# Kernel optimization log

Measured on AMD Instinct MI355X. Metric: run time of the kernel, lower is better.

The kernel has to match this reference:

```python
import jax, jax.numpy as jnp
import numpy as np

NUM_EXPERTS = 16
IN_FEATURES = 512
OUT_FEATURES = 512
N_TOKENS = 2048


def setup_inputs() -> dict:
    key = jax.random.key(0)
    k_x, k_idx, k_w, k_b = jax.random.split(key, 4)
    x = jax.random.normal(k_x, (N_TOKENS, IN_FEATURES), dtype=jnp.float32)
    indices = jax.random.randint(k_idx, (N_TOKENS,), 0, NUM_EXPERTS, dtype=jnp.int64)
    # nn.Linear default init: U(-1/sqrt(in), 1/sqrt(in)) for weight [out,in] and bias [out]
    bound = 1.0 / np.sqrt(IN_FEATURES)
    W = jax.random.uniform(k_w, (NUM_EXPERTS, OUT_FEATURES, IN_FEATURES),
                           minval=-bound, maxval=bound, dtype=jnp.float32)
    b = jax.random.uniform(k_b, (NUM_EXPERTS, OUT_FEATURES),
                           minval=-bound, maxval=bound, dtype=jnp.float32)
    return {"x": x, "indices": indices, "W": W, "b": b}


def reference(x, indices, W, b):
    # Faithful to SwitchLinear.forward: gather per-token expert weight/bias,
    # then per-token GEMV (batched matmul with a length-1 row dim).
    w_tok = W[indices]            # [N, out, in]  (naive per-token weight gather)
    b_tok = b[indices]            # [N, out]
    out = jnp.einsum('ni,noi->no', x, w_tok) + b_tok  # [N, out]
    return out
```

## Files before the change

### kernel.cpp

```cpp
#include <hip/hip_runtime.h>
#include <hip/hip_bf16.h>

#define NE    16
#define INF   512
#define OUTF  512
#define NT    2048
#define OTILE 64
#define TCH   32
#define NZ    2
#define WROWS OTILE
#define LSTRIDE 520

#define SZ_W   (WROWS * LSTRIDE * 2)
#define SZ_X   (TCH * LSTRIDE * 2)
#define SZ_LST ((NT + TCH) * 4)
#define SMEM_BYTES (SZ_W + SZ_X + SZ_LST + 32)

typedef __attribute__((ext_vector_type(4))) float f32x4;
typedef __attribute__((ext_vector_type(8))) short bf16x8;
typedef __attribute__((ext_vector_type(4))) short bf16x4;

__device__ inline short f2bf(float f) {
    union { __hip_bfloat16 h; short s; } u;
    u.h = __float2bfloat16(f);
    return u.s;
}

__device__ inline bf16x4 cvt4(f32x4 v) {
    bf16x4 r;
    r[0] = f2bf(v[0]); r[1] = f2bf(v[1]); r[2] = f2bf(v[2]); r[3] = f2bf(v[3]);
    return r;
}

__global__ __launch_bounds__(512, 2)
void switch_linear_kernel(const float* __restrict__ x,
                          const int* __restrict__ idx,
                          const float* __restrict__ W,
                          const float* __restrict__ bias,
                          float* __restrict__ out)
{
    extern __shared__ char smem[];
    short* s_W    = (short*)smem;
    short* s_X    = (short*)(smem + SZ_W);
    int*   s_list = (int*)(smem + SZ_W + SZ_X);
    int*   s_wcnt = (int*)(smem + SZ_W + SZ_X + SZ_LST);

    const int b   = blockIdx.x;
    const int e   = b & 15;
    const int oj  = (b >> 4) & 7;
    const int o0  = oj * OTILE;
    const int z   = b >> 7;
    const int tid = threadIdx.x;
    const int lane = tid & 63;
    const int wid  = tid >> 6;

    int iv[4];
#pragma unroll
    for (int it = 0; it < 4; ++it)
        iv[it] = idx[wid * 256 + it * 64 + lane];

    const float* wbase = W + ((size_t)e * OUTF + o0) * INF;
#pragma unroll
    for (int i = 0; i < 16; ++i) {
        const int ii = z ? ((i + 8) & 15) : i;
        const int li = tid + ii * 512;
        f32x4 v = ((const f32x4*)wbase)[li];
        const int row = li >> 7;
        const int col = (li * 4) & 511;
        *(bf16x4*)(&s_W[row * LSTRIDE + col]) = cvt4(v);
    }

    unsigned long long masks[4];
    int wtot = 0;
#pragma unroll
    for (int it = 0; it < 4; ++it) {
        const unsigned long long mk = __ballot(iv[it] == e);
        masks[it] = mk;
        wtot += __popcll(mk);
    }
    if (lane == 0) s_wcnt[wid] = wtot;
    __syncthreads();
    int base = 0;
#pragma unroll
    for (int w = 0; w < 8; ++w) { int c = s_wcnt[w]; if (w < wid) base += c; }
    const int cnt = s_wcnt[0] + s_wcnt[1] + s_wcnt[2] + s_wcnt[3]
                  + s_wcnt[4] + s_wcnt[5] + s_wcnt[6] + s_wcnt[7];
    const unsigned long long below = (1ull << lane) - 1ull;
    int run = base;
#pragma unroll
    for (int it = 0; it < 4; ++it) {
        const unsigned long long mk = masks[it];
        if (mk & (1ull << lane))
            s_list[run + __popcll(mk & below)] = wid * 256 + it * 64 + lane;
        run += __popcll(mk);
    }
    const int cnt_pad = (cnt + TCH - 1) & ~(TCH - 1);
    for (int i = cnt + tid; i < cnt_pad; i += 512) s_list[i] = -1;
    __syncthreads();
    if (cnt == 0) return;

    const int wt = wid >> 2;
    const int wo = wid & 3;
    const int lr = lane & 15;
    const int q  = lane >> 4;
    const int orow = o0 + wo * 16 + lr;

    bf16x8 bfr[16];
#pragma unroll
    for (int kk = 0; kk < 16; ++kk)
        bfr[kk] = *(const bf16x8*)(&s_W[(wo * 16 + lr) * LSTRIDE + kk * 32 + q * 8]);
    const float bv = bias[e * OUTF + orow];

    const int slot = tid >> 4;
    const int sub  = tid & 15;

    const int M = (cnt_pad - z * TCH + (NZ * TCH) - 1) / (NZ * TCH);
    if (M > 0) {
        int m0 = oj % M;
        for (int k = 0; k < M; ++k) {
            int m = m0 + k; if (m >= M) m -= M;
            const int cb = z * TCH + m * (NZ * TCH);

            int tok_s = s_list[cb + slot];
            if (tok_s < 0) tok_s = 0;
            const f32x4* xr = (const f32x4*)(x + (size_t)tok_s * INF);
#pragma unroll
            for (int i = 0; i < 8; ++i) {
                f32x4 v = xr[sub + i * 16];
                *(bf16x4*)(&s_X[slot * LSTRIDE + sub * 4 + i * 64]) = cvt4(v);
            }
            __syncthreads();

            f32x4 acc = {0.f, 0.f, 0.f, 0.f};
#pragma unroll
            for (int kk = 0; kk < 16; ++kk) {
                bf16x8 afr = *(const bf16x8*)(&s_X[(wt * 16 + lr) * LSTRIDE + kk * 32 + q * 8]);
                acc = __builtin_amdgcn_mfma_f32_16x16x32_bf16(afr, bfr[kk], acc, 0, 0, 0);
            }
#pragma unroll
            for (int j = 0; j < 4; ++j) {
                const int tok = s_list[cb + wt * 16 + q * 4 + j];
                if (tok >= 0) out[(size_t)tok * OUTF + orow] = acc[j] + bv;
            }
            __syncthreads();
        }
    }
}

extern "C" void kernel_launch(void* const* d_in, const int* in_sizes, int n_in,
                              void* d_out, int out_size, void* d_ws, size_t ws_size,
                              hipStream_t stream) {
    const float* x    = (const float*)d_in[0];
    const int*   idx  = (const int*)d_in[1];
    const float* W    = (const float*)d_in[2];
    const float* bias = (const float*)d_in[3];
    float* out = (float*)d_out;

    dim3 grid(NE * (OUTF / OTILE) * NZ);
    dim3 block(512);
    switch_linear_kernel<<<grid, block, SMEM_BYTES, stream>>>(x, idx, W, bias, out);
}
```

Baseline: 13.29 us.

## Double token chunk to 64 and restructure wave tiling over outputs

Raises the token chunk per iteration from 32 to 64 and remaps the 8 waves to 4 token groups by 2 output halves, so each wave runs two MFMAs per k-step and reads weight fragments from LDS instead of holding them in registers. The weight tile load is issued to registers before the routing ballot and converted into LDS afterwards, overlapping global latency with list construction. The z-dependent rotation of the weight-load order is dropped, and the trailing barrier is skipped on the last iteration. The intent is fewer loop iterations and barriers per block, traded against more LDS traffic and extra register pressure from the wreg and xreg arrays.

```diff
diff --git a/kernel.cpp b/kernel.cpp
--- a/kernel.cpp
+++ b/kernel.cpp
@@ -6,29 +6,29 @@
 #define OUTF  512
 #define NT    2048
 #define OTILE 64
-#define TCH   32
+#define TCH   64
 #define NZ    2
-#define WROWS OTILE
 #define LSTRIDE 520
 
-#define SZ_W   (WROWS * LSTRIDE * 2)
+#define SZ_W   (OTILE * LSTRIDE * 2)
 #define SZ_X   (TCH * LSTRIDE * 2)
 #define SZ_LST ((NT + TCH) * 4)
-#define SMEM_BYTES (SZ_W + SZ_X + SZ_LST + 32)
+#define SMEM_BYTES (SZ_W + SZ_X + SZ_LST + 64)
 
 typedef __attribute__((ext_vector_type(4))) float f32x4;
 typedef __attribute__((ext_vector_type(8))) short bf16x8;
 typedef __attribute__((ext_vector_type(4))) short bf16x4;
 
-__device__ inline short f2bf(float f) {
-    union { __hip_bfloat16 h; short s; } u;
+__device__ inline unsigned short f2bf(float f) {
+    union { __hip_bfloat16 h; unsigned short s; } u;
     u.h = __float2bfloat16(f);
     return u.s;
 }
 
 __device__ inline bf16x4 cvt4(f32x4 v) {
     bf16x4 r;
-    r[0] = f2bf(v[0]); r[1] = f2bf(v[1]); r[2] = f2bf(v[2]); r[3] = f2bf(v[3]);
+    r[0] = (short)f2bf(v[0]); r[1] = (short)f2bf(v[1]);
+    r[2] = (short)f2bf(v[2]); r[3] = (short)f2bf(v[3]);
     return r;
 }
 
@@ -60,15 +60,10 @@
         iv[it] = idx[wid * 256 + it * 64 + lane];
 
     const float* wbase = W + ((size_t)e * OUTF + o0) * INF;
+    f32x4 wreg[16];
 #pragma unroll
-    for (int i = 0; i < 16; ++i) {
-        const int ii = z ? ((i + 8) & 15) : i;
-        const int li = tid + ii * 512;
-        f32x4 v = ((const f32x4*)wbase)[li];
-        const int row = li >> 7;
-        const int col = (li * 4) & 511;
-        *(bf16x4*)(&s_W[row * LSTRIDE + col]) = cvt4(v);
-    }
+    for (int i = 0; i < 16; ++i)
+        wreg[i] = ((const f32x4*)wbase)[tid + i * 512];
 
     unsigned long long masks[4];
     int wtot = 0;
@@ -96,54 +91,68 @@
     }
     const int cnt_pad = (cnt + TCH - 1) & ~(TCH - 1);
     for (int i = cnt + tid; i < cnt_pad; i += 512) s_list[i] = -1;
+
+#pragma unroll
+    for (int i = 0; i < 16; ++i) {
+        const int li  = tid + i * 512;
+        const int row = li >> 7;
+        const int col = (li * 4) & 511;
+        *(bf16x4*)(&s_W[row * LSTRIDE + col]) = cvt4(wreg[i]);
+    }
     __syncthreads();
     if (cnt == 0) return;
 
-    const int wt = wid >> 2;
-    const int wo = wid & 3;
-    const int lr = lane & 15;
-    const int q  = lane >> 4;
-    const int orow = o0 + wo * 16 + lr;
+    const int wt  = wid >> 1;
+    const int wo2 = wid & 1;
+    const int lr  = lane & 15;
+    const int q   = lane >> 4;
+    const int or0 = o0 + wo2 * 32 + lr;
+    const float bv0 = bias[e * OUTF + or0];
+    const float bv1 = bias[e * OUTF + or0 + 16];
 
-    bf16x8 bfr[16];
+    const int slot = tid >> 3;
+    const int sub  = tid & 7;
+
+    const int nch = cnt_pad / TCH;
+    const int M = (nch - z + NZ - 1) / NZ;
+    if (M <= 0) return;
+    int m0 = oj % M;
+
+    for (int k = 0; k < M; ++k) {
+        int m = m0 + k; if (m >= M) m -= M;
+        const int cb = (z + m * NZ) * TCH;
+
+        int tok_s = s_list[cb + slot];
+        if (tok_s < 0) tok_s = 0;
+        const f32x4* xr = (const f32x4*)(x + (size_t)tok_s * INF);
+        f32x4 xreg[16];
 #pragma unroll
-    for (int kk = 0; kk < 16; ++kk)
-        bfr[kk] = *(const bf16x8*)(&s_W[(wo * 16 + lr) * LSTRIDE + kk * 32 + q * 8]);
-    const float bv = bias[e * OUTF + orow];
+        for (int i = 0; i < 16; ++i)
+            xreg[i] = xr[sub + i * 8];
+#pragma unroll
+        for (int i = 0; i < 16; ++i)
+            *(bf16x4*)(&s_X[slot * LSTRIDE + (sub + i * 8) * 4]) = cvt4(xreg[i]);
+        __syncthreads();
 
-    const int slot = tid >> 4;
-    const int sub  = tid & 15;
-
-    const int M = (cnt_pad - z * TCH + (NZ * TCH) - 1) / (NZ * TCH);
-    if (M > 0) {
-        int m0 = oj % M;
-        for (int k = 0; k < M; ++k) {
-            int m = m0 + k; if (m >= M) m -= M;
-            const int cb = z * TCH + m * (NZ * TCH);
-
-            int tok_s = s_list[cb + slot];
-            if (tok_s < 0) tok_s = 0;
-            const f32x4* xr = (const f32x4*)(x + (size_t)tok_s * INF);
+        f32x4 acc0 = {0.f, 0.f, 0.f, 0.f};
+        f32x4 acc1 = {0.f, 0.f, 0.f, 0.f};
 #pragma unroll
-            for (int i = 0; i < 8; ++i) {
-                f32x4 v = xr[sub + i * 16];
-                *(bf16x4*)(&s_X[slot * LSTRIDE + sub * 4 + i * 64]) = cvt4(v);
+        for (int kk = 0; kk < 16; ++kk) {
+            bf16x8 afr = *(const bf16x8*)(&s_X[(wt * 16 + lr) * LSTRIDE + kk * 32 + q * 8]);
+            bf16x8 b0  = *(const bf16x8*)(&s_W[(wo2 * 32 + lr) * LSTRIDE + kk * 32 + q * 8]);
+            bf16x8 b1  = *(const bf16x8*)(&s_W[(wo2 * 32 + 16 + lr) * LSTRIDE + kk * 32 + q * 8]);
+            acc0 = __builtin_amdgcn_mfma_f32_16x16x32_bf16(afr, b0, acc0, 0, 0, 0);
+            acc1 = __builtin_amdgcn_mfma_f32_16x16x32_bf16(afr, b1, acc1, 0, 0, 0);
+        }
+#pragma unroll
+        for (int j = 0; j < 4; ++j) {
+            const int tok = s_list[cb + wt * 16 + q * 4 + j];
+            if (tok >= 0) {
+                out[(size_t)tok * OUTF + or0]      = acc0[j] + bv0;
+                out[(size_t)tok * OUTF + or0 + 16] = acc1[j] + bv1;
             }
-            __syncthreads();
-
-            f32x4 acc = {0.f, 0.f, 0.f, 0.f};
-#pragma unroll
-            for (int kk = 0; kk < 16; ++kk) {
-                bf16x8 afr = *(const bf16x8*)(&s_X[(wt * 16 + lr) * LSTRIDE + kk * 32 + q * 8]);
-                acc = __builtin_amdgcn_mfma_f32_16x16x32_bf16(afr, bfr[kk], acc, 0, 0, 0);
-            }
-#pragma unroll
-            for (int j = 0; j < 4; ++j) {
-                const int tok = s_list[cb + wt * 16 + q * 4 + j];
-                if (tok >= 0) out[(size_t)tok * OUTF + orow] = acc[j] + bv;
-            }
-            __syncthreads();
         }
+        if (k != M - 1) __syncthreads();
     }
 }
 
```

New measurement: 14.73 us. +10.9%, slower.

## Double-buffer token chunk staging to overlap x loads with MFMA compute

Applied to the files above, without the earlier changes.

Adds a second LDS buffer for the bf16 token tile and prefetches the next chunk's x rows into registers while the current chunk runs its MFMA loop and output stores. The converted rows are then written into the alternate buffer between two barriers. This is meant to hide global load latency of x behind compute. In exchange it uses more LDS and registers, which may reduce occupancy at 512 threads with two blocks per CU, and each iteration still has two barriers.

```diff
diff --git a/kernel.cpp b/kernel.cpp
--- a/kernel.cpp
+++ b/kernel.cpp
@@ -8,27 +8,27 @@
 #define OTILE 64
 #define TCH   32
 #define NZ    2
-#define WROWS OTILE
 #define LSTRIDE 520
 
-#define SZ_W   (WROWS * LSTRIDE * 2)
+#define SZ_W   (OTILE * LSTRIDE * 2)
 #define SZ_X   (TCH * LSTRIDE * 2)
 #define SZ_LST ((NT + TCH) * 4)
-#define SMEM_BYTES (SZ_W + SZ_X + SZ_LST + 32)
+#define SMEM_BYTES (SZ_W + 2 * SZ_X + SZ_LST + 64)
 
 typedef __attribute__((ext_vector_type(4))) float f32x4;
 typedef __attribute__((ext_vector_type(8))) short bf16x8;
 typedef __attribute__((ext_vector_type(4))) short bf16x4;
 
-__device__ inline short f2bf(float f) {
-    union { __hip_bfloat16 h; short s; } u;
+__device__ inline unsigned short f2bf(float f) {
+    union { __hip_bfloat16 h; unsigned short s; } u;
     u.h = __float2bfloat16(f);
     return u.s;
 }
 
 __device__ inline bf16x4 cvt4(f32x4 v) {
     bf16x4 r;
-    r[0] = f2bf(v[0]); r[1] = f2bf(v[1]); r[2] = f2bf(v[2]); r[3] = f2bf(v[3]);
+    r[0] = (short)f2bf(v[0]); r[1] = (short)f2bf(v[1]);
+    r[2] = (short)f2bf(v[2]); r[3] = (short)f2bf(v[3]);
     return r;
 }
 
@@ -41,9 +41,10 @@
 {
     extern __shared__ char smem[];
     short* s_W    = (short*)smem;
-    short* s_X    = (short*)(smem + SZ_W);
-    int*   s_list = (int*)(smem + SZ_W + SZ_X);
-    int*   s_wcnt = (int*)(smem + SZ_W + SZ_X + SZ_LST);
+    short* s_X0   = (short*)(smem + SZ_W);
+    short* s_X1   = (short*)(smem + SZ_W + SZ_X);
+    int*   s_list = (int*)(smem + SZ_W + 2 * SZ_X);
+    int*   s_wcnt = (int*)(smem + SZ_W + 2 * SZ_X + SZ_LST);
 
     const int b   = blockIdx.x;
     const int e   = b & 15;
@@ -114,34 +115,60 @@
     const int slot = tid >> 4;
     const int sub  = tid & 15;
 
-    const int M = (cnt_pad - z * TCH + (NZ * TCH) - 1) / (NZ * TCH);
-    if (M > 0) {
-        int m0 = oj % M;
-        for (int k = 0; k < M; ++k) {
-            int m = m0 + k; if (m >= M) m -= M;
-            const int cb = z * TCH + m * (NZ * TCH);
+    const int nch = cnt_pad / TCH;
+    const int M = (nch - z + NZ - 1) / NZ;
+    if (M <= 0) return;
+    const int m0 = oj % M;
 
-            int tok_s = s_list[cb + slot];
+    {
+        const int cb = (z + m0 * NZ) * TCH;
+        int tok_s = s_list[cb + slot];
+        if (tok_s < 0) tok_s = 0;
+        const f32x4* xr = (const f32x4*)(x + (size_t)tok_s * INF);
+        f32x4 xreg[8];
+#pragma unroll
+        for (int i = 0; i < 8; ++i) xreg[i] = xr[sub + i * 16];
+#pragma unroll
+        for (int i = 0; i < 8; ++i)
+            *(bf16x4*)(&s_X0[slot * LSTRIDE + (sub + i * 16) * 4]) = cvt4(xreg[i]);
+    }
+    __syncthreads();
+
+    f32x4 xreg[8];
+    for (int k = 0; k < M; ++k) {
+        const int j  = (m0 + k) < M ? (m0 + k) : (m0 + k - M);
+        const int cb = (z + j * NZ) * TCH;
+        short* cbuf = (k & 1) ? s_X1 : s_X0;
+        short* nbuf = (k & 1) ? s_X0 : s_X1;
+
+        const bool more = (k + 1) < M;
+        if (more) {
+            const int jn  = (m0 + k + 1) < M ? (m0 + k + 1) : (m0 + k + 1 - M);
+            const int cbn = (z + jn * NZ) * TCH;
+            int tok_s = s_list[cbn + slot];
             if (tok_s < 0) tok_s = 0;
             const f32x4* xr = (const f32x4*)(x + (size_t)tok_s * INF);
 #pragma unroll
-            for (int i = 0; i < 8; ++i) {
-                f32x4 v = xr[sub + i * 16];
-                *(bf16x4*)(&s_X[slot * LSTRIDE + sub * 4 + i * 64]) = cvt4(v);
-            }
+            for (int i = 0; i < 8; ++i) xreg[i] = xr[sub + i * 16];
+        }
+
+        f32x4 acc = {0.f, 0.f, 0.f, 0.f};
+#pragma unroll
+        for (int kk = 0; kk < 16; ++kk) {
+            bf16x8 afr = *(const bf16x8*)(&cbuf[(wt * 16 + lr) * LSTRIDE + kk * 32 + q * 8]);
+            acc = __builtin_amdgcn_mfma_f32_16x16x32_bf16(afr, bfr[kk], acc, 0, 0, 0);
+        }
+#pragma unroll
+        for (int j4 = 0; j4 < 4; ++j4) {
+            const int tok = s_list[cb + wt * 16 + q * 4 + j4];
+            if (tok >= 0) out[(size_t)tok * OUTF + orow] = acc[j4] + bv;
+        }
+
+        if (more) {
             __syncthreads();
-
-            f32x4 acc = {0.f, 0.f, 0.f, 0.f};
 #pragma unroll
-            for (int kk = 0; kk < 16; ++kk) {
-                bf16x8 afr = *(const bf16x8*)(&s_X[(wt * 16 + lr) * LSTRIDE + kk * 32 + q * 8]);
-                acc = __builtin_amdgcn_mfma_f32_16x16x32_bf16(afr, bfr[kk], acc, 0, 0, 0);
-            }
-#pragma unroll
-            for (int j = 0; j < 4; ++j) {
-                const int tok = s_list[cb + wt * 16 + q * 4 + j];
-                if (tok >= 0) out[(size_t)tok * OUTF + orow] = acc[j] + bv;
-            }
+            for (int i = 0; i < 8; ++i)
+                *(bf16x4*)(&nbuf[slot * LSTRIDE + (sub + i * 16) * 4]) = cvt4(xreg[i]);
             __syncthreads();
         }
     }
```

Result: no change. 13.20 us (-0.7%).
